# Kernel tuning notes

Measured on AMD Instinct MI355X. Metric: run time of the kernel, lower is better.

Reference implementation:

```python
import jax, jax.numpy as jnp
import numpy as np

# The original module performs bit-exact IEEE754 FP64 arithmetic via spiking
# neurons; we enable x64 so intermediates match the FP64 pipeline exactly.
jax.config.update("jax_enable_x64", True)

B, S, D = 2, 2048, 1024
NBITS = 32

_SHIFTS = jnp.arange(31, -1, -1, dtype=jnp.uint32)  # MSB-first, matching pulse[..., i] = bit (31-i)


def float32_to_pulse(vals):
    """float32 array [...] -> pulse bits [..., 32], MSB first, as float32 0/1."""
    u = jax.lax.bitcast_convert_type(vals, jnp.uint32)
    bits = (u[..., None] >> _SHIFTS) & jnp.uint32(1)
    return bits.astype(jnp.float32)


def pulse_to_float32(pulse):
    """pulse bits [..., 32] (float 0/1, MSB first) -> float32 array [...]."""
    bits = pulse.astype(jnp.uint32)
    u = jnp.sum(bits << _SHIFTS, axis=-1, dtype=jnp.uint32)
    return jax.lax.bitcast_convert_type(u, jnp.float32)


def _gelu_exact_bits(x_pulse):
    # FP32 pulses -> FP32 value -> FP64 (FP32ToFP64Converter is exact)
    v = pulse_to_float32(x_pulse).astype(jnp.float64)
    # with tanh(z) = (exp(2z) - 1) / (exp(2z) + 1), exactly as the spiking chain computes it.
    x_sq = v * v
    x_cubed = x_sq * v
    inner = v + jnp.float64(0.044715) * x_cubed
    z = jnp.float64(0.7978845608028654) * inner
    e2z = jnp.exp(jnp.float64(2.0) * z)
    tanh_z = (e2z - jnp.float64(1.0)) / (e2z + jnp.float64(1.0))
    res64 = jnp.float64(0.5) * (v * (jnp.float64(1.0) + tanh_z))
    # FP64ToFP32Converter: round-to-nearest down-cast, then re-encode as pulses
    return float32_to_pulse(res64.astype(jnp.float32))


def setup_inputs() -> dict:
    key = jax.random.key(0)
    vals = jax.random.normal(key, (B, S, D), dtype=jnp.float32)  # realistic activations
    x = float32_to_pulse(vals)  # [B, S, D, 32] float32 0/1 pulses
    return {"x": x}


def reference(x) -> jnp.ndarray:
    return _gelu_exact_bits(x)
```

## Files before the change

kernel.cpp:

```cpp
#include <hip/hip_runtime.h>


__global__ __launch_bounds__(256) void spike_gelu_kernel(const float* __restrict__ in,
                                                         float* __restrict__ out,
                                                         int nvals) {
    int v = blockIdx.x * blockDim.x + threadIdx.x;
    if (v >= nvals) return;

    const float4* __restrict__ in4 = reinterpret_cast<const float4*>(in) + (size_t)v * 8;
    float4* __restrict__ out4 = reinterpret_cast<float4*>(out) + (size_t)v * 8;

    unsigned int u = 0u;
#pragma unroll
    for (int k = 0; k < 8; ++k) {
        float4 f = in4[k];
        unsigned int b0 = (f.x != 0.0f) ? 1u : 0u;
        unsigned int b1 = (f.y != 0.0f) ? 1u : 0u;
        unsigned int b2 = (f.z != 0.0f) ? 1u : 0u;
        unsigned int b3 = (f.w != 0.0f) ? 1u : 0u;
        u |= (b0 << (31 - 4 * k)) | (b1 << (30 - 4 * k)) |
             (b2 << (29 - 4 * k)) | (b3 << (28 - 4 * k));
    }

    {
#pragma clang fp contract(off)
        float xf = __uint_as_float(u);
        double vd = (double)xf;
        double x_sq = vd * vd;
        double x_cubed = x_sq * vd;
        double inner = vd + 0.044715 * x_cubed;
        double z = 0.7978845608028654 * inner;
        double e2z = exp(2.0 * z);
        double tanh_z = (e2z - 1.0) / (e2z + 1.0);
        double res64 = 0.5 * (vd * (1.0 + tanh_z));
        float rf = (float)res64;
        u = __float_as_uint(rf);
    }

#pragma unroll
    for (int k = 0; k < 8; ++k) {
        float4 o;
        o.x = (float)((u >> (31 - 4 * k)) & 1u);
        o.y = (float)((u >> (30 - 4 * k)) & 1u);
        o.z = (float)((u >> (29 - 4 * k)) & 1u);
        o.w = (float)((u >> (28 - 4 * k)) & 1u);
        out4[k] = o;
    }
}

extern "C" void kernel_launch(void* const* d_in, const int* in_sizes, int n_in,
                              void* d_out, int out_size, void* d_ws, size_t ws_size,
                              hipStream_t stream) {
    const float* x = (const float*)d_in[0];
    float* out = (float*)d_out;
    int nvals = out_size / 32;
    int block = 256;
    int grid = (nvals + block - 1) / block;
    spike_gelu_kernel<<<grid, block, 0, stream>>>(x, out, nvals);
}
```

Before: 886.9 us.

## Coalesce pulse loads and stores across wave lanes using shuffles

Before, each thread read and wrote its own 128-byte run of pulses, so the lanes of a wave hit strided addresses. Now each wave handles a contiguous block: on each of 8 iterations the lanes load consecutive float4s, build partial bit words, OR-reduce them across groups of 8 lanes with xor shuffles, and the owning lane keeps the full word. The output step broadcasts each word back with shuffles so the stores are coalesced too. This adds shuffle instructions and now reads the 0/1 floats through an unsigned cast instead of a compare against zero.

```diff
diff --git a/kernel.cpp b/kernel.cpp
--- a/kernel.cpp
+++ b/kernel.cpp
@@ -4,22 +4,31 @@
 __global__ __launch_bounds__(256) void spike_gelu_kernel(const float* __restrict__ in,
                                                          float* __restrict__ out,
                                                          int nvals) {
-    int v = blockIdx.x * blockDim.x + threadIdx.x;
-    if (v >= nvals) return;
+    const int tid  = blockIdx.x * blockDim.x + threadIdx.x;
+    const int lane = threadIdx.x & 63;
+    const int wave = tid >> 6;
+    if (wave * 64 >= nvals) return;
 
-    const float4* __restrict__ in4 = reinterpret_cast<const float4*>(in) + (size_t)v * 8;
-    float4* __restrict__ out4 = reinterpret_cast<float4*>(out) + (size_t)v * 8;
+    const size_t base4 = (size_t)wave * 512;
+    const float4* __restrict__ in4 = reinterpret_cast<const float4*>(in) + base4;
+    float4* __restrict__ out4      = reinterpret_cast<float4*>(out) + base4;
+
+    const int c  = lane & 7;
+    const int s0 = 31 - 4 * c;
 
     unsigned int u = 0u;
 #pragma unroll
-    for (int k = 0; k < 8; ++k) {
-        float4 f = in4[k];
-        unsigned int b0 = (f.x != 0.0f) ? 1u : 0u;
-        unsigned int b1 = (f.y != 0.0f) ? 1u : 0u;
-        unsigned int b2 = (f.z != 0.0f) ? 1u : 0u;
-        unsigned int b3 = (f.w != 0.0f) ? 1u : 0u;
-        u |= (b0 << (31 - 4 * k)) | (b1 << (30 - 4 * k)) |
-             (b2 << (29 - 4 * k)) | (b3 << (28 - 4 * k));
+    for (int r = 0; r < 8; ++r) {
+        float4 f = in4[r * 64 + lane];
+        unsigned int partial =
+              ((unsigned int)f.x << s0)
+            | ((unsigned int)f.y << (s0 - 1))
+            | ((unsigned int)f.z << (s0 - 2))
+            | ((unsigned int)f.w << (s0 - 3));
+        partial |= __shfl_xor(partial, 1);
+        partial |= __shfl_xor(partial, 2);
+        partial |= __shfl_xor(partial, 4);
+        if (c == r) u = partial;
     }
 
     {
@@ -38,13 +47,14 @@
     }
 
 #pragma unroll
-    for (int k = 0; k < 8; ++k) {
+    for (int r = 0; r < 8; ++r) {
+        unsigned int w = (unsigned int)__shfl((int)u, (lane & 56) | r);
         float4 o;
-        o.x = (float)((u >> (31 - 4 * k)) & 1u);
-        o.y = (float)((u >> (30 - 4 * k)) & 1u);
-        o.z = (float)((u >> (29 - 4 * k)) & 1u);
-        o.w = (float)((u >> (28 - 4 * k)) & 1u);
-        out4[k] = o;
+        o.x = (float)((w >> s0) & 1u);
+        o.y = (float)((w >> (s0 - 1)) & 1u);
+        o.z = (float)((w >> (s0 - 2)) & 1u);
+        o.w = (float)((w >> (s0 - 3)) & 1u);
+        out4[r * 64 + lane] = o;
     }
 }
 
```

New measurement: 836.3 us. 5.7% less time.

## Pack and unpack pulse bits with wave ballots and readlanes for coalesced access

Applied to the files above, without the earlier changes.

Each wave now reads 64 consecutive floats per step (dword loads, fully coalesced across lanes) and forms each value's 32-bit word with __ballot, then scatters words back via readlane for the output. Before, each thread issued eight strided float4 loads and stores. The new layout gives contiguous per-instruction memory access but replaces 8 vector loads with 32 scalar loads and adds 64 readlanes per thread. It also assumes nvals is a multiple of 64 and no partial waves.

```diff
diff --git a/kernel.cpp b/kernel.cpp
--- a/kernel.cpp
+++ b/kernel.cpp
@@ -4,22 +4,25 @@
 __global__ __launch_bounds__(256) void spike_gelu_kernel(const float* __restrict__ in,
                                                          float* __restrict__ out,
                                                          int nvals) {
-    int v = blockIdx.x * blockDim.x + threadIdx.x;
-    if (v >= nvals) return;
+    const int tid  = blockIdx.x * blockDim.x + threadIdx.x;
+    const int lane = threadIdx.x & 63;
+    const int wave = tid >> 6;
+    if (wave * 64 >= nvals) return;
 
-    const float4* __restrict__ in4 = reinterpret_cast<const float4*>(in) + (size_t)v * 8;
-    float4* __restrict__ out4 = reinterpret_cast<float4*>(out) + (size_t)v * 8;
+    const int lx = lane ^ 31;
+    const size_t base = (size_t)wave * 2048;
+    const float* __restrict__ ip = in  + base + lx;
+    float*       __restrict__ op = out + base + lx;
 
     unsigned int u = 0u;
 #pragma unroll
-    for (int k = 0; k < 8; ++k) {
-        float4 f = in4[k];
-        unsigned int b0 = (f.x != 0.0f) ? 1u : 0u;
-        unsigned int b1 = (f.y != 0.0f) ? 1u : 0u;
-        unsigned int b2 = (f.z != 0.0f) ? 1u : 0u;
-        unsigned int b3 = (f.w != 0.0f) ? 1u : 0u;
-        u |= (b0 << (31 - 4 * k)) | (b1 << (30 - 4 * k)) |
-             (b2 << (29 - 4 * k)) | (b3 << (28 - 4 * k));
+    for (int r = 0; r < 32; ++r) {
+        float f = ip[64 * r];
+        unsigned long long m = __ballot(f != 0.0f);
+        unsigned int lo = (unsigned int)m;
+        unsigned int hi = (unsigned int)(m >> 32);
+        if (lane == 2 * r)     u = lo;
+        if (lane == 2 * r + 1) u = hi;
     }
 
     {
@@ -37,14 +40,14 @@
         u = __float_as_uint(rf);
     }
 
+    const unsigned int sl = (unsigned int)(lane & 31);
+    const bool hi_half = (lane >= 32);
 #pragma unroll
-    for (int k = 0; k < 8; ++k) {
-        float4 o;
-        o.x = (float)((u >> (31 - 4 * k)) & 1u);
-        o.y = (float)((u >> (30 - 4 * k)) & 1u);
-        o.z = (float)((u >> (29 - 4 * k)) & 1u);
-        o.w = (float)((u >> (28 - 4 * k)) & 1u);
-        out4[k] = o;
+    for (int r = 0; r < 32; ++r) {
+        unsigned int s0 = __builtin_amdgcn_readlane(u, 2 * r);
+        unsigned int s1 = __builtin_amdgcn_readlane(u, 2 * r + 1);
+        unsigned int w  = hi_half ? s1 : s0;
+        op[64 * r] = (float)((w >> sl) & 1u);
     }
 }
 
```

Result: faster. 836.4 us (-5.7%).
